# Kernel tuning notes

Hardware: AMD Instinct MI355X
Metric: run time of the kernel (lower is better)

Reference implementation:

```python
import jax, jax.numpy as jnp
import numpy as np

EMB = 1024
HEADS = 16

def setup_inputs() -> dict:
    key = jax.random.key(0)
    ks = jax.random.split(key, 5)
    s = 1.0 / np.sqrt(EMB)
    x = jax.random.normal(ks[0], (2, 2048, EMB), dtype=jnp.float32)
    W_qkv = jax.random.normal(ks[1], (EMB, 3 * EMB), dtype=jnp.float32) * s
    b_qkv = jnp.zeros((3 * EMB,), dtype=jnp.float32)
    W_out = jax.random.normal(ks[2], (EMB, EMB), dtype=jnp.float32) * s
    b_out = jnp.zeros((EMB,), dtype=jnp.float32)
    return {"x": x, "W_qkv": W_qkv, "b_qkv": b_qkv, "W_out": W_out, "b_out": b_out}

def reference(x, W_qkv, b_qkv, W_out, b_out):
    B, N, C = x.shape
    H = HEADS
    D = C // H
    qkv = x @ W_qkv + b_qkv                      # [B,N,3C]
    qkv = qkv.reshape(B, N, 3, H, D)
    q, k, v = (qkv[:, :, i].transpose(0, 2, 1, 3) for i in range(3))  # [B,H,N,D]
    # NOTE: original scales by C**-0.5 (full embed dim), not head dim
    scale = C ** (-0.5)
    attn = jnp.einsum('bhnd,bhmd->bhnm', q, k) * scale
    attn = jax.nn.softmax(attn, axis=-1)
    out = jnp.einsum('bhnm,bhmd->bhnd', attn, v)  # [B,H,N,D]
    out = out.transpose(0, 2, 1, 3).reshape(B, N, C)
    return out @ W_out + b_out
```

## Files before the change

### kernel.cpp

```cpp
#include <hip/hip_runtime.h>
#include <hip/hip_bf16.h>
#include <cstdint>
#include <cstddef>

typedef __bf16 bf16;
typedef __bf16 bf16x4 __attribute__((ext_vector_type(4)));
typedef __bf16 bf16x8 __attribute__((ext_vector_type(8)));
typedef float f32x4 __attribute__((ext_vector_type(4)));

#define LOG2E 1.4426950408889634f
#define QSCALE (0.03125f * LOG2E)
#define PSHIFT 8.0f

#define GLD16(gp, lp)                                                              \
  __builtin_amdgcn_global_load_lds((__attribute__((address_space(1))) void*)(gp),  \
                                   (__attribute__((address_space(3))) void*)(lp),  \
                                   16, 0, 0)


__global__ void k_cvt_bf16(const float* __restrict__ in, bf16* __restrict__ out) {
  int i = (blockIdx.x * 256 + threadIdx.x) * 8;
  const float4* p = (const float4*)(in + i);
  float4 a = p[0], b = p[1];
  bf16x8 o;
  o[0] = (bf16)a.x; o[1] = (bf16)a.y; o[2] = (bf16)a.z; o[3] = (bf16)a.w;
  o[4] = (bf16)b.x; o[5] = (bf16)b.y; o[6] = (bf16)b.z; o[7] = (bf16)b.w;
  *(bf16x8*)(out + i) = o;
}

__global__ void k_transpose_cvt(const float* __restrict__ in, bf16* __restrict__ out,
                                int R, int C) {
  __shared__ float t[32][33];
  int c0 = blockIdx.x * 32, r0 = blockIdx.y * 32;
#pragma unroll
  for (int i = 0; i < 4; i++)
    t[threadIdx.y + i * 8][threadIdx.x] =
        in[(size_t)(r0 + threadIdx.y + i * 8) * C + c0 + threadIdx.x];
  __syncthreads();
#pragma unroll
  for (int i = 0; i < 4; i++)
    out[(size_t)(c0 + threadIdx.y + i * 8) * R + r0 + threadIdx.x] =
        (bf16)t[threadIdx.x][threadIdx.y + i * 8];
}

template <int EPI>
__global__ __launch_bounds__(256, 2) void k_gemm_bt(
    const bf16* __restrict__ A, const bf16* __restrict__ Bt,
    const float* __restrict__ bias, float* __restrict__ outF,
    bf16* __restrict__ qb, bf16* __restrict__ kb, bf16* __restrict__ vb) {
  __shared__ __align__(16) bf16 As[128 * 32];
  __shared__ __align__(16) bf16 Bs[128 * 32];
  const int tid = threadIdx.x;
  const int lane = tid & 63, w = tid >> 6;
  const int quad = lane >> 4, l16 = lane & 15;
  const int wm = (w >> 1) * 64, wn = (w & 1) * 64;
  const int bm = blockIdx.y * 128, bn = blockIdx.x * 128;
  f32x4 acc[4][4] = {};

  for (int kt = 0; kt < 1024; kt += 32) {
    __syncthreads();
#pragma unroll
    for (int p = 0; p < 2; p++) {
      int idx = p * 256 + tid;
      int row = idx >> 2, bq = idx & 3;
      int gb = (bq - ((row >> 1) & 3)) & 3;
      GLD16(A + (size_t)(bm + row) * 1024 + kt + gb * 8, As + idx * 8);
      GLD16(Bt + (size_t)(bn + row) * 1024 + kt + gb * 8, Bs + idx * 8);
    }
    __syncthreads();

    bf16x8 af[4], bfr[4];
#pragma unroll
    for (int mi = 0; mi < 4; mi++) {
      int row = wm + mi * 16 + l16;
      int bq = (quad + ((row >> 1) & 3)) & 3;
      af[mi] = *(const bf16x8*)(As + row * 32 + bq * 8);
    }
#pragma unroll
    for (int ni = 0; ni < 4; ni++) {
      int row = wn + ni * 16 + l16;
      int bq = (quad + ((row >> 1) & 3)) & 3;
      bfr[ni] = *(const bf16x8*)(Bs + row * 32 + bq * 8);
    }
#pragma unroll
    for (int mi = 0; mi < 4; mi++)
#pragma unroll
      for (int ni = 0; ni < 4; ni++)
        acc[mi][ni] =
            __builtin_amdgcn_mfma_f32_16x16x32_bf16(af[mi], bfr[ni], acc[mi][ni], 0, 0, 0);
  }

#pragma unroll
  for (int ni = 0; ni < 4; ni++) {
    int col = bn + wn + ni * 16 + l16;
    float bv = bias[col];
    if (EPI == 1) {
#pragma unroll
      for (int mi = 0; mi < 4; mi++)
#pragma unroll
        for (int r = 0; r < 4; r++) {
          int row = bm + wm + mi * 16 + quad * 4 + r;
          outF[(size_t)row * 1024 + col] = acc[mi][ni][r] + bv;
        }
    } else {
      int which = col >> 10, cc = col & 1023;
      int h = cc >> 6, d = cc & 63;
      if (which == 2) {
#pragma unroll
        for (int mi = 0; mi < 4; mi++) {
          int rowb = bm + wm + mi * 16 + quad * 4;
          int b = rowb >> 11, n0 = rowb & 2047;
          bf16x4 vv;
#pragma unroll
          for (int r = 0; r < 4; r++) vv[r] = (bf16)(acc[mi][ni][r] + bv);
          *(bf16x4*)(vb + ((size_t)(b * 16 + h) * 64 + d) * 2048 + n0) = vv;
        }
      } else {
#pragma unroll
        for (int mi = 0; mi < 4; mi++)
#pragma unroll
          for (int r = 0; r < 4; r++) {
            int row = bm + wm + mi * 16 + quad * 4 + r;
            int b = row >> 11, n = row & 2047;
            float v = acc[mi][ni][r] + bv;
            if (which == 0)
              qb[((size_t)(b * 16 + h) * 2048 + n) * 64 + d] = (bf16)(v * QSCALE);
            else
              kb[((size_t)(b * 16 + h) * 2048 + n) * 64 + d] = (bf16)v;
          }
      }
    }
  }
}

__global__ __launch_bounds__(256, 3) void k_flash(
    const bf16* __restrict__ Q, const bf16* __restrict__ K,
    const bf16* __restrict__ V, bf16* __restrict__ O) {
  __shared__ __align__(16) bf16 Kt[2][64 * 64];
  __shared__ __align__(16) bf16 Vt[2][64 * 64];
  __shared__ __align__(16) bf16 Pb[4][32 * 64];
  const int tid = threadIdx.x;
  const int lane = tid & 63, w = tid >> 6;
  const int quad = lane >> 4, l16 = lane & 15;
  const int bh = blockIdx.y, qt = blockIdx.x;
  const bf16* qh = Q + (size_t)bh * 2048 * 64;
  const bf16* kh = K + (size_t)bh * 2048 * 64;
  const bf16* vh = V + (size_t)bh * 64 * 2048;

  bf16x8 qf[2][2];
#pragma unroll
  for (int mi = 0; mi < 2; mi++)
#pragma unroll
    for (int kc = 0; kc < 2; kc++)
      qf[mi][kc] = *(const bf16x8*)(qh + (size_t)(qt * 128 + w * 32 + mi * 16 + l16) * 64 +
                                    kc * 32 + quad * 8);

  bf16x8 ones;
#pragma unroll
  for (int j = 0; j < 8; j++) ones[j] = (bf16)1.0f;

  f32x4 o[2][4] = {};
  f32x4 lacc[2] = {};

  bf16* pw = &Pb[w][0];

  auto stage = [&](int kt2, int buf) {
#pragma unroll
    for (int p = 0; p < 2; p++) {
      int idx = p * 256 + tid;
      int row = idx >> 3, bq = idx & 7, gb = bq ^ (row & 7);
      GLD16(kh + (size_t)(kt2 * 64 + row) * 64 + gb * 8, &Kt[buf][idx * 8]);
      GLD16(vh + (size_t)row * 2048 + kt2 * 64 + gb * 8, &Vt[buf][idx * 8]);
    }
  };

  stage(0, 0);

  for (int kt2 = 0; kt2 < 32; kt2++) {
    const int p = kt2 & 1;
    __syncthreads();
    if (kt2 < 31) stage(kt2 + 1, p ^ 1);
    const bf16* Kb = &Kt[p][0];
    const bf16* Vb = &Vt[p][0];

    f32x4 s[2][4];
#pragma unroll
    for (int nj = 0; nj < 4; nj++) {
      int row = nj * 16 + l16;
      bf16x8 kf0 = *(const bf16x8*)(Kb + row * 64 + ((quad ^ (row & 7)) << 3));
      bf16x8 kf1 = *(const bf16x8*)(Kb + row * 64 + (((4 + quad) ^ (row & 7)) << 3));
#pragma unroll
      for (int mi = 0; mi < 2; mi++) {
        f32x4 t = {-PSHIFT, -PSHIFT, -PSHIFT, -PSHIFT};
        t = __builtin_amdgcn_mfma_f32_16x16x32_bf16(kf0, qf[mi][0], t, 0, 0, 0);
        t = __builtin_amdgcn_mfma_f32_16x16x32_bf16(kf1, qf[mi][1], t, 0, 0, 0);
        s[mi][nj] = t;
      }
    }

#pragma unroll
    for (int mi = 0; mi < 2; mi++) {
      bf16* pr = pw + (mi * 16 + l16) * 64;
#pragma unroll
      for (int nj = 0; nj < 4; nj++) {
        bf16x4 pk;
#pragma unroll
        for (int r = 0; r < 4; r++) pk[r] = (bf16)__builtin_amdgcn_exp2f(s[mi][nj][r]);
        int blk = (nj * 2 + (quad >> 1)) ^ (l16 & 7);
        *(bf16x4*)(pr + blk * 8 + (quad & 1) * 4) = pk;
      }
    }

#pragma unroll
    for (int kc = 0; kc < 2; kc++) {
      bf16x8 pf[2];
#pragma unroll
      for (int mi = 0; mi < 2; mi++) {
        pf[mi] = *(const bf16x8*)(pw + (mi * 16 + l16) * 64 + (((kc * 4 + quad) ^ (l16 & 7)) << 3));
        lacc[mi] = __builtin_amdgcn_mfma_f32_16x16x32_bf16(ones, pf[mi], lacc[mi], 0, 0, 0);
      }
#pragma unroll
      for (int nd = 0; nd < 4; nd++) {
        int row = nd * 16 + l16;
        bf16x8 vf = *(const bf16x8*)(Vb + row * 64 + (((kc * 4 + quad) ^ (row & 7)) << 3));
        o[0][nd] = __builtin_amdgcn_mfma_f32_16x16x32_bf16(vf, pf[0], o[0][nd], 0, 0, 0);
        o[1][nd] = __builtin_amdgcn_mfma_f32_16x16x32_bf16(vf, pf[1], o[1][nd], 0, 0, 0);
      }
    }
  }

  const int b = bh >> 4, h = bh & 15;
#pragma unroll
  for (int mi = 0; mi < 2; mi++) {
    float inv = 1.0f / lacc[mi][0];
    int n = qt * 128 + w * 32 + mi * 16 + l16;
#pragma unroll
    for (int nd = 0; nd < 4; nd++) {
      bf16x4 ov;
#pragma unroll
      for (int r = 0; r < 4; r++) ov[r] = (bf16)(o[mi][nd][r] * inv);
      int c = h * 64 + nd * 16 + quad * 4;
      *(bf16x4*)(O + ((size_t)b * 2048 + n) * 1024 + c) = ov;
    }
  }
}


extern "C" void kernel_launch(void* const* d_in, const int* in_sizes, int n_in,
                              void* d_out, int out_size, void* d_ws, size_t ws_size,
                              hipStream_t stream) {
  (void)in_sizes; (void)n_in; (void)out_size; (void)ws_size;
  const float* x    = (const float*)d_in[0];
  const float* Wqkv = (const float*)d_in[1];
  const float* bqkv = (const float*)d_in[2];
  const float* Wout = (const float*)d_in[3];
  const float* bout = (const float*)d_in[4];
  float* out = (float*)d_out;

  char* ws = (char*)d_ws;
  size_t off = 0;
  auto take = [&](size_t bytes) {
    char* p = ws + off;
    off += (bytes + 255) & ~(size_t)255;
    return p;
  };
  bf16* xb   = (bf16*)take((size_t)4096 * 1024 * 2);
  bf16* wqT  = (bf16*)take((size_t)3072 * 1024 * 2);
  bf16* woT  = (bf16*)take((size_t)1024 * 1024 * 2);
  bf16* qbuf = (bf16*)take((size_t)32 * 2048 * 64 * 2);
  bf16* kbuf = (bf16*)take((size_t)32 * 2048 * 64 * 2);
  bf16* vbuf = (bf16*)take((size_t)32 * 2048 * 64 * 2);
  bf16* aout = (bf16*)take((size_t)4096 * 1024 * 2);

  k_cvt_bf16<<<4096 * 1024 / (256 * 8), 256, 0, stream>>>(x, xb);
  k_transpose_cvt<<<dim3(96, 32), dim3(32, 8), 0, stream>>>(Wqkv, wqT, 1024, 3072);
  k_transpose_cvt<<<dim3(32, 32), dim3(32, 8), 0, stream>>>(Wout, woT, 1024, 1024);
  k_gemm_bt<0><<<dim3(24, 32), 256, 0, stream>>>(xb, wqT, bqkv, nullptr, qbuf, kbuf, vbuf);
  k_flash<<<dim3(16, 32), 256, 0, stream>>>(qbuf, kbuf, vbuf, aout);
  k_gemm_bt<1><<<dim3(8, 32), 256, 0, stream>>>(aout, woT, bout, out, nullptr, nullptr, nullptr);
}
```

Before: 194.5 us.

## Merge prep kernels into one launch and halve flash query tile per block

Merges the x conversion and both weight transpose-conversions into a single k_prep launch that dispatches on block index, cutting two kernel launches. The flash kernel now gives each wave 16 query rows instead of 32, so a block covers 64 queries, the grid doubles to 1024 blocks and the P scratch in LDS shrinks. Launch bounds rise to 4 blocks per CU for more occupancy. The trade-off is that each K/V tile loaded into LDS is reused across half as many queries, doubling K/V staging traffic.

```diff
diff --git a/kernel.cpp b/kernel.cpp
--- a/kernel.cpp
+++ b/kernel.cpp
@@ -17,30 +17,40 @@
                                    (__attribute__((address_space(3))) void*)(lp),  \
                                    16, 0, 0)
 
-
-__global__ void k_cvt_bf16(const float* __restrict__ in, bf16* __restrict__ out) {
-  int i = (blockIdx.x * 256 + threadIdx.x) * 8;
-  const float4* p = (const float4*)(in + i);
-  float4 a = p[0], b = p[1];
-  bf16x8 o;
-  o[0] = (bf16)a.x; o[1] = (bf16)a.y; o[2] = (bf16)a.z; o[3] = (bf16)a.w;
-  o[4] = (bf16)b.x; o[5] = (bf16)b.y; o[6] = (bf16)b.z; o[7] = (bf16)b.w;
-  *(bf16x8*)(out + i) = o;
-}
-
-__global__ void k_transpose_cvt(const float* __restrict__ in, bf16* __restrict__ out,
-                                int R, int C) {
+__global__ void k_prep(const float* __restrict__ x, const float* __restrict__ Wqkv,
+                       const float* __restrict__ Wout, bf16* __restrict__ xb,
+                       bf16* __restrict__ wqT, bf16* __restrict__ woT) {
+  const int blk = blockIdx.x, tid = threadIdx.x;
+  if (blk < 2048) {
+    int i = (blk * 256 + tid) * 8;
+    const float4* p = (const float4*)(x + i);
+    float4 a = p[0], b = p[1];
+    bf16x8 o;
+    o[0] = (bf16)a.x; o[1] = (bf16)a.y; o[2] = (bf16)a.z; o[3] = (bf16)a.w;
+    o[4] = (bf16)b.x; o[5] = (bf16)b.y; o[6] = (bf16)b.z; o[7] = (bf16)b.w;
+    *(bf16x8*)(xb + i) = o;
+    return;
+  }
+  const float* in;
+  bf16* out;
+  int R = 1024, C, bx, by;
+  if (blk < 2048 + 3072) {
+    in = Wqkv; out = wqT; C = 3072;
+    bx = (blk - 2048) % 96; by = (blk - 2048) / 96;
+  } else {
+    in = Wout; out = woT; C = 1024;
+    bx = (blk - 5120) % 32; by = (blk - 5120) / 32;
+  }
   __shared__ float t[32][33];
-  int c0 = blockIdx.x * 32, r0 = blockIdx.y * 32;
+  const int tx = tid & 31, ty = tid >> 5;
+  int c0 = bx * 32, r0 = by * 32;
 #pragma unroll
   for (int i = 0; i < 4; i++)
-    t[threadIdx.y + i * 8][threadIdx.x] =
-        in[(size_t)(r0 + threadIdx.y + i * 8) * C + c0 + threadIdx.x];
+    t[ty + i * 8][tx] = in[(size_t)(r0 + ty + i * 8) * C + c0 + tx];
   __syncthreads();
 #pragma unroll
   for (int i = 0; i < 4; i++)
-    out[(size_t)(c0 + threadIdx.y + i * 8) * R + r0 + threadIdx.x] =
-        (bf16)t[threadIdx.x][threadIdx.y + i * 8];
+    out[(size_t)(c0 + ty + i * 8) * R + r0 + tx] = (bf16)t[tx][ty + i * 8];
 }
 
 template <int EPI>
@@ -133,12 +143,12 @@
   }
 }
 
-__global__ __launch_bounds__(256, 3) void k_flash(
+__global__ __launch_bounds__(256, 4) void k_flash(
     const bf16* __restrict__ Q, const bf16* __restrict__ K,
     const bf16* __restrict__ V, bf16* __restrict__ O) {
   __shared__ __align__(16) bf16 Kt[2][64 * 64];
   __shared__ __align__(16) bf16 Vt[2][64 * 64];
-  __shared__ __align__(16) bf16 Pb[4][32 * 64];
+  __shared__ __align__(16) bf16 Pb[4][16 * 64];
   const int tid = threadIdx.x;
   const int lane = tid & 63, w = tid >> 6;
   const int quad = lane >> 4, l16 = lane & 15;
@@ -147,20 +157,17 @@
   const bf16* kh = K + (size_t)bh * 2048 * 64;
   const bf16* vh = V + (size_t)bh * 64 * 2048;
 
-  bf16x8 qf[2][2];
-#pragma unroll
-  for (int mi = 0; mi < 2; mi++)
-#pragma unroll
-    for (int kc = 0; kc < 2; kc++)
-      qf[mi][kc] = *(const bf16x8*)(qh + (size_t)(qt * 128 + w * 32 + mi * 16 + l16) * 64 +
-                                    kc * 32 + quad * 8);
+  bf16x8 qf[2];
+#pragma unroll
+  for (int kc = 0; kc < 2; kc++)
+    qf[kc] = *(const bf16x8*)(qh + (size_t)(qt * 64 + w * 16 + l16) * 64 + kc * 32 + quad * 8);
 
   bf16x8 ones;
 #pragma unroll
   for (int j = 0; j < 8; j++) ones[j] = (bf16)1.0f;
 
-  f32x4 o[2][4] = {};
-  f32x4 lacc[2] = {};
+  f32x4 o[4] = {};
+  f32x4 lacc = {};
 
   bf16* pw = &Pb[w][0];
 
@@ -183,29 +190,25 @@
     const bf16* Kb = &Kt[p][0];
     const bf16* Vb = &Vt[p][0];
 
-    f32x4 s[2][4];
+    f32x4 s[4];
 #pragma unroll
     for (int nj = 0; nj < 4; nj++) {
       int row = nj * 16 + l16;
       bf16x8 kf0 = *(const bf16x8*)(Kb + row * 64 + ((quad ^ (row & 7)) << 3));
       bf16x8 kf1 = *(const bf16x8*)(Kb + row * 64 + (((4 + quad) ^ (row & 7)) << 3));
-#pragma unroll
-      for (int mi = 0; mi < 2; mi++) {
-        f32x4 t = {-PSHIFT, -PSHIFT, -PSHIFT, -PSHIFT};
-        t = __builtin_amdgcn_mfma_f32_16x16x32_bf16(kf0, qf[mi][0], t, 0, 0, 0);
-        t = __builtin_amdgcn_mfma_f32_16x16x32_bf16(kf1, qf[mi][1], t, 0, 0, 0);
-        s[mi][nj] = t;
-      }
-    }
-
-#pragma unroll
-    for (int mi = 0; mi < 2; mi++) {
-      bf16* pr = pw + (mi * 16 + l16) * 64;
+      f32x4 t = {-PSHIFT, -PSHIFT, -PSHIFT, -PSHIFT};
+      t = __builtin_amdgcn_mfma_f32_16x16x32_bf16(kf0, qf[0], t, 0, 0, 0);
+      t = __builtin_amdgcn_mfma_f32_16x16x32_bf16(kf1, qf[1], t, 0, 0, 0);
+      s[nj] = t;
+    }
+
+    {
+      bf16* pr = pw + l16 * 64;
 #pragma unroll
       for (int nj = 0; nj < 4; nj++) {
         bf16x4 pk;
 #pragma unroll
-        for (int r = 0; r < 4; r++) pk[r] = (bf16)__builtin_amdgcn_exp2f(s[mi][nj][r]);
+        for (int r = 0; r < 4; r++) pk[r] = (bf16)__builtin_amdgcn_exp2f(s[nj][r]);
         int blk = (nj * 2 + (quad >> 1)) ^ (l16 & 7);
         *(bf16x4*)(pr + blk * 8 + (quad & 1) * 4) = pk;
       }
@@ -213,35 +216,28 @@
 
 #pragma unroll
     for (int kc = 0; kc < 2; kc++) {
-      bf16x8 pf[2];
-#pragma unroll
-      for (int mi = 0; mi < 2; mi++) {
-        pf[mi] = *(const bf16x8*)(pw + (mi * 16 + l16) * 64 + (((kc * 4 + quad) ^ (l16 & 7)) << 3));
-        lacc[mi] = __builtin_amdgcn_mfma_f32_16x16x32_bf16(ones, pf[mi], lacc[mi], 0, 0, 0);
-      }
+      bf16x8 pf =
+          *(const bf16x8*)(pw + l16 * 64 + (((kc * 4 + quad) ^ (l16 & 7)) << 3));
+      lacc = __builtin_amdgcn_mfma_f32_16x16x32_bf16(ones, pf, lacc, 0, 0, 0);
 #pragma unroll
       for (int nd = 0; nd < 4; nd++) {
         int row = nd * 16 + l16;
         bf16x8 vf = *(const bf16x8*)(Vb + row * 64 + (((kc * 4 + quad) ^ (row & 7)) << 3));
-        o[0][nd] = __builtin_amdgcn_mfma_f32_16x16x32_bf16(vf, pf[0], o[0][nd], 0, 0, 0);
-        o[1][nd] = __builtin_amdgcn_mfma_f32_16x16x32_bf16(vf, pf[1], o[1][nd], 0, 0, 0);
+        o[nd] = __builtin_amdgcn_mfma_f32_16x16x32_bf16(vf, pf, o[nd], 0, 0, 0);
       }
     }
   }
 
   const int b = bh >> 4, h = bh & 15;
-#pragma unroll
-  for (int mi = 0; mi < 2; mi++) {
-    float inv = 1.0f / lacc[mi][0];
-    int n = qt * 128 + w * 32 + mi * 16 + l16;
-#pragma unroll
-    for (int nd = 0; nd < 4; nd++) {
-      bf16x4 ov;
-#pragma unroll
-      for (int r = 0; r < 4; r++) ov[r] = (bf16)(o[mi][nd][r] * inv);
-      int c = h * 64 + nd * 16 + quad * 4;
-      *(bf16x4*)(O + ((size_t)b * 2048 + n) * 1024 + c) = ov;
-    }
+  float inv = 1.0f / lacc[0];
+  int n = qt * 64 + w * 16 + l16;
+#pragma unroll
+  for (int nd = 0; nd < 4; nd++) {
+    bf16x4 ov;
+#pragma unroll
+    for (int r = 0; r < 4; r++) ov[r] = (bf16)(o[nd][r] * inv);
+    int c = h * 64 + nd * 16 + quad * 4;
+    *(bf16x4*)(O + ((size_t)b * 2048 + n) * 1024 + c) = ov;
   }
 }
 
@@ -272,10 +268,8 @@
   bf16* vbuf = (bf16*)take((size_t)32 * 2048 * 64 * 2);
   bf16* aout = (bf16*)take((size_t)4096 * 1024 * 2);
 
-  k_cvt_bf16<<<4096 * 1024 / (256 * 8), 256, 0, stream>>>(x, xb);
-  k_transpose_cvt<<<dim3(96, 32), dim3(32, 8), 0, stream>>>(Wqkv, wqT, 1024, 3072);
-  k_transpose_cvt<<<dim3(32, 32), dim3(32, 8), 0, stream>>>(Wout, woT, 1024, 1024);
+  k_prep<<<6144, 256, 0, stream>>>(x, Wqkv, Wout, xb, wqT, woT);
   k_gemm_bt<0><<<dim3(24, 32), 256, 0, stream>>>(xb, wqT, bqkv, nullptr, qbuf, kbuf, vbuf);
-  k_flash<<<dim3(16, 32), 256, 0, stream>>>(qbuf, kbuf, vbuf, aout);
+  k_flash<<<dim3(32, 32), 256, 0, stream>>>(qbuf, kbuf, vbuf, aout);
   k_gemm_bt<1><<<dim3(8, 32), 256, 0, stream>>>(aout, woT, bout, out, nullptr, nullptr, nullptr);
 }
```

After: 190.6 us. -2.0%, faster.
